# Performance work log

Hardware: AMD Instinct MI355X
Metric: run time of the kernel (lower is better)

## Reference

```python
import jax, jax.numpy as jnp
import numpy as np

B, C, F, N = 8, 128, 16, 512  # batch, in_channels, frames, num_nodes


def setup_inputs() -> dict:
    key = jax.random.key(0)
    k = jax.random.split(key, 6)
    return {
        # uniform(0,1) -> all entries nonzero -> complete graph with self-loops
        "Y": jax.random.uniform(k[0], (B, F, N, N), dtype=jnp.float32),
        "infos": jax.random.normal(k[1], (B, C, F, N), dtype=jnp.float32),
        # denseLayer: Linear(3C, C) -> weight [C, 3C], bias [C]
        "W_dense": jax.random.normal(k[2], (C, 3 * C), dtype=jnp.float32) / np.sqrt(3 * C).astype(np.float32),
        "b_dense": jax.random.normal(k[3], (C,), dtype=jnp.float32) * 0.01,
        # NodeApplyModule linear: Linear(C, C)
        "W_node": jax.random.normal(k[4], (C, C), dtype=jnp.float32) / np.sqrt(C).astype(np.float32),
        "b_node": jax.random.normal(k[5], (C,), dtype=jnp.float32) * 0.01,
    }


def reference(Y, infos, W_dense, b_dense, W_node, b_node):
    Bs, Cs, Fs, Ns = infos.shape
    # graph_update: frame 0 uses Y[:,0], frames 1..11 use Y[:,1], frames >11 use Y[:,2]
    frames = jnp.arange(Fs)
    y_idx = jnp.where(frames == 0, 0, jnp.where(frames <= 11, 1, 2))
    M = (Y[:, y_idx] != 0).astype(infos.dtype)          # [B,F,N,N] adjacency mask (u->v)
    X = jnp.transpose(infos, (0, 2, 3, 1))               # [B,F,N,C] node features

    # msg(u,v) = X[u] * (cat[X[u], X[v], X[u]-X[v]] @ W_dense.T + b_dense)
    # Linear is separable: gate(u,v) = S[u] + D[v] + b_dense with
    #   S = X @ (W1+W3).T, D = X @ (W2-W3).T
    W1, W2, W3 = jnp.split(W_dense, 3, axis=1)           # each [C,C]
    S = jnp.einsum('bfnc,dc->bfnd', X, W1 + W3)
    D = jnp.einsum('bfnc,dc->bfnd', X, W2 - W3)

    # mean over incoming edges u of msg(u,v):
    #   sum_u M[u,v] * X[u]*S[u]  +  (sum_u M[u,v]*X[u]) * (D[v]+b)
    A1 = jnp.einsum('bfuv,bfuc->bfvc', M, X * S)
    A2 = jnp.einsum('bfuv,bfuc->bfvc', M, X)
    deg = jnp.maximum(M.sum(axis=2), 1.0)[..., None]     # in-degree [B,F,N,1]
    agg = (A1 + A2 * (D + b_dense)) / deg

    # NodeApplyModule: relu(Linear(agg))
    h = jax.nn.relu(jnp.einsum('bfnc,oc->bfno', agg, W_node) + b_node)
    # reshape/permute to [B, C, F, N] and final relu (idempotent after relu)
    return jax.nn.relu(jnp.transpose(h, (0, 3, 1, 2)))
```

## Files before the change

### kernel.cpp

```cpp
#include <hip/hip_runtime.h>
#include <hip/hip_bf16.h>

#define B_ 8
#define C_ 128
#define F_ 16
#define N_ 512
#define CAP_ (N_ * N_)

typedef __attribute__((ext_vector_type(8))) short bf16x8;
typedef __attribute__((ext_vector_type(4))) float f32x4;

#define MFMA(a, b, c) __builtin_amdgcn_mfma_f32_16x16x32_bf16((a), (b), (c), 0, 0, 0)
#define SWZ(x) ((x) ^ ((((x) >> 8) & 7) << 4))

__device__ __forceinline__ ushort f2bf(float x) {
    union { __hip_bfloat16 h; ushort u; } cv;
    cv.h = __float2bfloat16(x);
    return cv.u;
}

__global__ __launch_bounds__(256) void k_prep(
    const float* __restrict__ Y, const float* __restrict__ Wd, const float* __restrict__ Wn,
    float* __restrict__ deg, int* __restrict__ cnt, int* __restrict__ list,
    float* __restrict__ Wsum, float* __restrict__ Wdiff, float* __restrict__ WsumT,
    ushort* __restrict__ WdT_bf, float* __restrict__ WnT)
{
    int t = threadIdx.x;
    if (blockIdx.y == 8) {
        for (int i = blockIdx.x * 256 + t; i < C_ * C_; i += 24 * 256) {
            int d = i >> 7, c = i & 127;
            const float* row = Wd + (size_t)d * (3 * C_);
            float w1 = row[c], w2 = row[C_ + c], w3 = row[2 * C_ + c];
            float ws = w1 + w3, wdf = w2 - w3;
            Wsum[i] = ws;
            Wdiff[i] = wdf;
            WsumT[(size_t)c * C_ + d] = ws;
            WdT_bf[(size_t)c * C_ + d] = f2bf(wdf);
            WnT[i] = Wn[(size_t)(i & 127) * C_ + (i >> 7)];
        }
        return;
    }
    __shared__ float red0[256], red1[256];
    int bg = blockIdx.x, vc = blockIdx.y;
    int b = bg / 3, g = bg % 3;
    int p = t & 31, q = t >> 5;
    int v = vc * 64 + p * 2;
    const float* Yp = Y + ((size_t)b * F_ + g) * N_ * N_;
    float d0 = 0.f, d1 = 0.f;
    #pragma unroll 4
    for (int i = 0; i < 64; ++i) {
        int u = q * 64 + i;
        float2 a = *(const float2*)(Yp + (size_t)u * N_ + v);
        if (a.x == 0.f) {
            int idx = atomicAdd(&cnt[bg], 1);
            list[(size_t)bg * CAP_ + idx] = (u << 9) | v;
        } else d0 += 1.f;
        if (a.y == 0.f) {
            int idx = atomicAdd(&cnt[bg], 1);
            list[(size_t)bg * CAP_ + idx] = (u << 9) | (v + 1);
        } else d1 += 1.f;
    }
    red0[t] = d0;
    red1[t] = d1;
    __syncthreads();
    if (t < 32) {
        float s0 = 0.f, s1 = 0.f;
        #pragma unroll
        for (int qq = 0; qq < 8; ++qq) { s0 += red0[qq * 32 + t]; s1 += red1[qq * 32 + t]; }
        deg[(size_t)bg * N_ + vc * 64 + t * 2]     = s0;
        deg[(size_t)bg * N_ + vc * 64 + t * 2 + 1] = s1;
    }
}

__global__ __launch_bounds__(256) void k_gram(
    const float* __restrict__ infos, const float* __restrict__ WsumT,
    float* __restrict__ A1row, float* __restrict__ A2row)
{
    __shared__ float smf[8448];
    __shared__ float red[256];
    short* Xs = (short*)smf;
    float* Gl = smf;
    int bf = blockIdx.x, nh = blockIdx.y, t = threadIdx.x;
    int b = bf >> 4, f = bf & 15;
    const float* Xg = infos + ((size_t)b * C_ * F_ + f) * N_;

    float a2p0 = 0.f, a2p1 = 0.f, a2p2 = 0.f, a2p3 = 0.f;
    float4 pre0, pre1, pre2, pre3;
    int sc = t >> 3, suq = t & 7;

    auto LOADREG = [&](int ks) {
        int u0 = ks * 32;
        const float* pbase = Xg + (size_t)sc * (F_ * N_) + u0 + suq * 4;
        pre0 = *(const float4*)(pbase);
        pre1 = *(const float4*)(pbase + 32 * (F_ * N_));
        pre2 = *(const float4*)(pbase + 64 * (F_ * N_));
        pre3 = *(const float4*)(pbase + 96 * (F_ * N_));
    };
    auto WRITELDS = [&](int buf) {
        short* dst = &Xs[buf * 5120 + sc * 40 + suq * 4];
        float4 xs[4] = {pre0, pre1, pre2, pre3};
        #pragma unroll
        for (int it = 0; it < 4; ++it) {
            float4 x = xs[it];
            float s4 = x.x + x.y + x.z + x.w;
            if (it == 0) a2p0 += s4; else if (it == 1) a2p1 += s4;
            else if (it == 2) a2p2 += s4; else a2p3 += s4;
            short4 h;
            h.x = (short)f2bf(x.x); h.y = (short)f2bf(x.y);
            h.z = (short)f2bf(x.z); h.w = (short)f2bf(x.w);
            *(short4*)(dst + it * 32 * 40) = h;
        }
    };

    int l = t & 63, w = t >> 6;
    int r = l & 15, q = l >> 4;
    f32x4 acc[2][4];
    #pragma unroll
    for (int mi = 0; mi < 2; ++mi)
        #pragma unroll
        for (int ni = 0; ni < 4; ++ni) acc[mi][ni] = (f32x4){0.f, 0.f, 0.f, 0.f};

    LOADREG(0);
    WRITELDS(0);
    for (int ks = 0; ks < 16; ++ks) {
        __syncthreads();
        if (ks < 15) LOADREG(ks + 1);
        const short* Xb = &Xs[(ks & 1) * 5120];
        bf16x8 a0 = *(const bf16x8*)&Xb[(w * 32 + r) * 40 + q * 8];
        bf16x8 a1 = *(const bf16x8*)&Xb[(w * 32 + 16 + r) * 40 + q * 8];
        bf16x8 b0 = *(const bf16x8*)&Xb[(nh * 64 + 0  + r) * 40 + q * 8];
        bf16x8 b1 = *(const bf16x8*)&Xb[(nh * 64 + 16 + r) * 40 + q * 8];
        bf16x8 b2 = *(const bf16x8*)&Xb[(nh * 64 + 32 + r) * 40 + q * 8];
        bf16x8 b3 = *(const bf16x8*)&Xb[(nh * 64 + 48 + r) * 40 + q * 8];
        acc[0][0] = MFMA(a0, b0, acc[0][0]);
        acc[0][1] = MFMA(a0, b1, acc[0][1]);
        acc[0][2] = MFMA(a0, b2, acc[0][2]);
        acc[0][3] = MFMA(a0, b3, acc[0][3]);
        acc[1][0] = MFMA(a1, b0, acc[1][0]);
        acc[1][1] = MFMA(a1, b1, acc[1][1]);
        acc[1][2] = MFMA(a1, b2, acc[1][2]);
        acc[1][3] = MFMA(a1, b3, acc[1][3]);
        if (ks < 15) WRITELDS((ks + 1) & 1);
    }
    __syncthreads();
    #pragma unroll
    for (int mi = 0; mi < 2; ++mi)
        #pragma unroll
        for (int ni = 0; ni < 4; ++ni) {
            int cb = w * 32 + mi * 16 + q * 4;
            int dl = ni * 16 + r;
            #pragma unroll
            for (int j = 0; j < 4; ++j) Gl[(cb + j) * 66 + dl] = acc[mi][ni][j];
        }
    __syncthreads();
    {
        int dl = t & 63, cq = t >> 6;
        float pacc = 0.f;
        #pragma unroll 8
        for (int i = 0; i < 32; ++i) {
            int c = cq * 32 + i;
            pacc += WsumT[(size_t)c * C_ + nh * 64 + dl] * Gl[c * 66 + dl];
        }
        red[t] = pacc;
    }
    __syncthreads();
    if (t < 64)
        A1row[(size_t)bf * C_ + nh * 64 + t] = red[t] + red[t + 64] + red[t + 128] + red[t + 192];
    if (nh == 0) {
        #pragma unroll
        for (int it = 0; it < 4; ++it) {
            float v2 = (it == 0) ? a2p0 : (it == 1) ? a2p1 : (it == 2) ? a2p2 : a2p3;
            v2 += __shfl_xor(v2, 1);
            v2 += __shfl_xor(v2, 2);
            v2 += __shfl_xor(v2, 4);
            if ((t & 7) == 0) A2row[(size_t)bf * C_ + it * 32 + (t >> 3)] = v2;
        }
    }
}

__global__ __launch_bounds__(256) void k_meff(
    const float* __restrict__ A1row, const float* __restrict__ A2row,
    const float* __restrict__ Wn, const float* __restrict__ WnT,
    const ushort* __restrict__ WdT_bf, const float* __restrict__ bd,
    ushort* __restrict__ Meff_bf, float* __restrict__ c0all)
{
    __shared__ ushort Zl[16384];
    __shared__ ushort Wl[16384];
    __shared__ float A2l[C_], El[C_];
    int bf = blockIdx.x, t = threadIdx.x;
    if (t < C_) {
        float a2 = A2row[(size_t)bf * C_ + t];
        A2l[t] = a2;
        El[t] = A1row[(size_t)bf * C_ + t] + a2 * bd[t];
    }
    __syncthreads();
    #pragma unroll
    for (int it = 0; it < 8; ++it) {
        int idx = it * 256 + t;
        int rowi = idx >> 4, ch = idx & 15;
        bf16x8 wv = *(const bf16x8*)&WdT_bf[(size_t)rowi * C_ + ch * 8];
        *(bf16x8*)((char*)Wl + SWZ(rowi * 256 + ch * 16)) = wv;
        const float4 w0 = *(const float4*)&Wn[(size_t)rowi * C_ + ch * 8];
        const float4 w1 = *(const float4*)&Wn[(size_t)rowi * C_ + ch * 8 + 4];
        bf16x8 z;
        z[0] = (short)f2bf(w0.x * A2l[ch * 8 + 0]);
        z[1] = (short)f2bf(w0.y * A2l[ch * 8 + 1]);
        z[2] = (short)f2bf(w0.z * A2l[ch * 8 + 2]);
        z[3] = (short)f2bf(w0.w * A2l[ch * 8 + 3]);
        z[4] = (short)f2bf(w1.x * A2l[ch * 8 + 4]);
        z[5] = (short)f2bf(w1.y * A2l[ch * 8 + 5]);
        z[6] = (short)f2bf(w1.z * A2l[ch * 8 + 6]);
        z[7] = (short)f2bf(w1.w * A2l[ch * 8 + 7]);
        *(bf16x8*)((char*)Zl + SWZ(rowi * 256 + ch * 16)) = z;
    }
    __syncthreads();
    int l = t & 63, w = t >> 6, r = l & 15, q = l >> 4;
    f32x4 acc[2][8];
    #pragma unroll
    for (int mi = 0; mi < 2; ++mi)
        #pragma unroll
        for (int ni = 0; ni < 8; ++ni) acc[mi][ni] = (f32x4){0.f, 0.f, 0.f, 0.f};
    #pragma unroll
    for (int ks = 0; ks < 4; ++ks) {
        int ko = ks * 64 + q * 16;
        bf16x8 a0 = *(const bf16x8*)((char*)Zl + SWZ((w * 32 + r) * 256 + ko));
        bf16x8 a1 = *(const bf16x8*)((char*)Zl + SWZ((w * 32 + 16 + r) * 256 + ko));
        #pragma unroll
        for (int ni = 0; ni < 8; ++ni) {
            bf16x8 bb = *(const bf16x8*)((char*)Wl + SWZ((ni * 16 + r) * 256 + ko));
            acc[0][ni] = MFMA(a0, bb, acc[0][ni]);
            acc[1][ni] = MFMA(a1, bb, acc[1][ni]);
        }
    }
    __syncthreads();
    #pragma unroll
    for (int mi = 0; mi < 2; ++mi)
        #pragma unroll
        for (int ni = 0; ni < 8; ++ni) {
            int o = w * 32 + mi * 16 + q * 4;
            int c = ni * 16 + r;
            #pragma unroll
            for (int j = 0; j < 4; ++j) Zl[(o + j) * C_ + c] = f2bf(acc[mi][ni][j]);
        }
    __syncthreads();
    #pragma unroll
    for (int it = 0; it < 8; ++it) {
        int idx = it * 256 + t;
        int rowi = idx >> 4, ch = idx & 15;
        *(bf16x8*)&Meff_bf[(size_t)bf * 16384 + rowi * C_ + ch * 8] =
            *(const bf16x8*)&Zl[rowi * C_ + ch * 8];
    }
    if (t < C_) {
        float s = 0.f;
        for (int c = 0; c < C_; ++c) s += WnT[(size_t)c * C_ + t] * El[c];
        c0all[(size_t)bf * C_ + t] = s;
    }
}

__global__ __launch_bounds__(256) void k_final(
    const float* __restrict__ infos, const ushort* __restrict__ Meff_bf,
    const float* __restrict__ c0all, const float* __restrict__ deg,
    const int* __restrict__ cnt, const int* __restrict__ list,
    const float* __restrict__ Wsum, const float* __restrict__ Wdiff,
    const float* __restrict__ Wn, const float* __restrict__ bd, const float* __restrict__ bn,
    float* __restrict__ out)
{
    __shared__ char arena[49152];
    ushort* Ml = (ushort*)arena;
    ushort* Xv = (ushort*)(arena + 32768);
    float*  Sl = (float*)arena;
    __shared__ float Xu[C_], Xvf[C_], NC[C_], corrv[C_];
    int bf = blockIdx.x, vb = blockIdx.y, t = threadIdx.x;
    int b = bf >> 4, f = bf & 15;
    int g = (f == 0) ? 0 : ((f <= 11) ? 1 : 2);
    int bg = b * 3 + g;
    int v0 = vb * 64;
    const float* Xg = infos + ((size_t)b * C_ * F_ + f) * N_;

    #pragma unroll
    for (int it = 0; it < 8; ++it) {
        int idx = it * 256 + t;
        int o = idx >> 4, ch = idx & 15;
        bf16x8 mv = *(const bf16x8*)&Meff_bf[(size_t)bf * 16384 + o * C_ + ch * 8];
        *(bf16x8*)((char*)Ml + SWZ(o * 256 + ch * 16)) = mv;
    }
    #pragma unroll
    for (int it = 0; it < 4; ++it) {
        int idx = it * 256 + t;
        int cp = idx >> 4, vq = idx & 15;
        const float* r0 = Xg + (size_t)(2 * cp) * (F_ * N_) + v0 + vq * 4;
        const float* r1 = r0 + (F_ * N_);
        float4 x0 = *(const float4*)r0;
        float4 x1 = *(const float4*)r1;
        float e0[4] = {x0.x, x0.y, x0.z, x0.w};
        float e1[4] = {x1.x, x1.y, x1.z, x1.w};
        #pragma unroll
        for (int j = 0; j < 4; ++j) {
            int vloc = vq * 4 + j;
            unsigned word = (unsigned)f2bf(e0[j]) | ((unsigned)f2bf(e1[j]) << 16);
            *(unsigned*)((char*)Xv + SWZ(vloc * 256 + cp * 4)) = word;
        }
    }
    __syncthreads();

    int l = t & 63, w = t >> 6, r = l & 15, q = l >> 4;
    f32x4 acc[2][4];
    #pragma unroll
    for (int mi = 0; mi < 2; ++mi)
        #pragma unroll
        for (int ni = 0; ni < 4; ++ni) acc[mi][ni] = (f32x4){0.f, 0.f, 0.f, 0.f};
    #pragma unroll
    for (int ks = 0; ks < 4; ++ks) {
        int ko = ks * 64 + q * 16;
        bf16x8 a0 = *(const bf16x8*)((char*)Ml + SWZ((w * 32 + r) * 256 + ko));
        bf16x8 a1 = *(const bf16x8*)((char*)Ml + SWZ((w * 32 + 16 + r) * 256 + ko));
        #pragma unroll
        for (int nt = 0; nt < 4; ++nt) {
            bf16x8 bb = *(const bf16x8*)((char*)Xv + SWZ((nt * 16 + r) * 256 + ko));
            acc[0][nt] = MFMA(a0, bb, acc[0][nt]);
            acc[1][nt] = MFMA(a1, bb, acc[1][nt]);
        }
    }

    int nz = cnt[bg];
    for (int e = 0; e < nz; ++e) {
        int p = list[(size_t)bg * CAP_ + e];
        int u = p >> 9, v = p & 511;
        if ((v >> 6) != vb) continue;
        int vloc = v - v0;
        __syncthreads();
        if (t < C_) {
            Xu[t]  = Xg[(size_t)t * (F_ * N_) + u];
            Xvf[t] = Xg[(size_t)t * (F_ * N_) + v];
        }
        __syncthreads();
        if (t < C_) {
            float s = 0.f, dv = 0.f;
            const float* wsr = Wsum + (size_t)t * C_;
            const float* wdr = Wdiff + (size_t)t * C_;
            for (int c = 0; c < C_; ++c) { s += wsr[c] * Xu[c]; dv += wdr[c] * Xvf[c]; }
            NC[t] = Xu[t] * (s + dv + bd[t]);
        }
        __syncthreads();
        if (t < C_) {
            float s = 0.f;
            const float* wnr = Wn + (size_t)t * C_;
            for (int c = 0; c < C_; ++c) s += wnr[c] * NC[c];
            corrv[t] = s;
        }
        __syncthreads();
        int ntv = vloc >> 4;
        #pragma unroll
        for (int nt = 0; nt < 4; ++nt) {
            if (nt == ntv && r == (vloc & 15)) {
                #pragma unroll
                for (int mi = 0; mi < 2; ++mi)
                    #pragma unroll
                    for (int j = 0; j < 4; ++j)
                        acc[mi][nt][j] -= corrv[w * 32 + mi * 16 + q * 4 + j];
            }
        }
    }

    float c0v[2][4], bnv[2][4];
    #pragma unroll
    for (int mi = 0; mi < 2; ++mi)
        #pragma unroll
        for (int j = 0; j < 4; ++j) {
            int o = w * 32 + mi * 16 + q * 4 + j;
            c0v[mi][j] = c0all[(size_t)bf * C_ + o];
            bnv[mi][j] = bn[o];
        }
    __syncthreads();
    #pragma unroll
    for (int nt = 0; nt < 4; ++nt) {
        int v = v0 + nt * 16 + r;
        float dg = fmaxf(deg[(size_t)bg * N_ + v], 1.f);
        #pragma unroll
        for (int mi = 0; mi < 2; ++mi) {
            int o = w * 32 + mi * 16 + q * 4;
            #pragma unroll
            for (int j = 0; j < 4; ++j) {
                float val = fmaxf((acc[mi][nt][j] + c0v[mi][j]) / dg + bnv[mi][j], 0.f);
                Sl[(o + j) * 66 + nt * 16 + r] = val;
            }
        }
    }
    __syncthreads();
    {
        int o = t >> 1, half = t & 1;
        float* src = &Sl[o * 66 + half * 32];
        float* dst = &out[((size_t)b * C_ + o) * (F_ * N_) + (size_t)f * N_ + v0 + half * 32];
        #pragma unroll
        for (int j = 0; j < 8; ++j)
            *(float4*)(dst + j * 4) = *(const float4*)(src + j * 4);
    }
}

extern "C" void kernel_launch(void* const* d_in, const int* in_sizes, int n_in,
                              void* d_out, int out_size, void* d_ws, size_t ws_size,
                              hipStream_t stream)
{
    const float* Y     = (const float*)d_in[0];
    const float* infos = (const float*)d_in[1];
    const float* Wd    = (const float*)d_in[2];
    const float* bd    = (const float*)d_in[3];
    const float* Wn    = (const float*)d_in[4];
    const float* bn    = (const float*)d_in[5];
    float* out = (float*)d_out;
    float* ws  = (float*)d_ws;

    float*  deg     = ws;
    int*    cnt     = (int*)(ws + 12288);
    float*  A1row   = ws + 12320;
    float*  A2row   = A1row + 16384;
    float*  Wsum    = A2row + 16384;
    float*  Wdiff   = Wsum + 16384;
    float*  WsumT   = Wdiff + 16384;
    float*  WnT     = WsumT + 16384;
    float*  c0all   = WnT + 16384;
    ushort* WdT_bf  = (ushort*)(c0all + 16384);
    ushort* Meff_bf = (ushort*)(c0all + 16384 + 8192);
    int*    list    = (int*)(c0all + 16384 + 8192 + 1048576);

    hipMemsetAsync(cnt, 0, 32 * sizeof(int), stream);
    k_prep<<<dim3(24, 9), 256, 0, stream>>>(Y, Wd, Wn, deg, cnt, list,
                                            Wsum, Wdiff, WsumT, WdT_bf, WnT);
    k_gram<<<dim3(B_ * F_, 2), 256, 0, stream>>>(infos, WsumT, A1row, A2row);
    k_meff<<<B_ * F_, 256, 0, stream>>>(A1row, A2row, Wn, WnT, WdT_bf, bd, Meff_bf, c0all);
    k_final<<<dim3(B_ * F_, 8), 256, 0, stream>>>(infos, Meff_bf, c0all, deg, cnt, list,
                                                  Wsum, Wdiff, Wn, bd, bn, out);
}
```

Measured before the change: 284.1 us.

## Fuse gram and Meff kernels into one 512-thread block per frame

Merges the Gram-matrix/A1/A2 kernel and the Meff kernel into a single 512-thread kernel per (batch, frame). A1 and A2 are reduced in shared memory instead of round-tripping through global memory, which removes one launch. WdT and Meff operands are now read straight from global memory instead of being staged in LDS. The final kernel likewise reads Meff directly from global, shrinking its LDS arena, which may help occupancy but adds uncoalesced global loads. The fused kernel runs only 128 blocks, so the Gram work is no longer split across two blocks per frame.

```diff
diff --git a/kernel.cpp b/kernel.cpp
--- a/kernel.cpp
+++ b/kernel.cpp
@@ -72,136 +72,90 @@
     }
 }
 
-__global__ __launch_bounds__(256) void k_gram(
+__global__ __launch_bounds__(512) void k_gram_meff(
     const float* __restrict__ infos, const float* __restrict__ WsumT,
-    float* __restrict__ A1row, float* __restrict__ A2row)
-{
-    __shared__ float smf[8448];
-    __shared__ float red[256];
-    short* Xs = (short*)smf;
-    float* Gl = smf;
-    int bf = blockIdx.x, nh = blockIdx.y, t = threadIdx.x;
-    int b = bf >> 4, f = bf & 15;
-    const float* Xg = infos + ((size_t)b * C_ * F_ + f) * N_;
-
-    float a2p0 = 0.f, a2p1 = 0.f, a2p2 = 0.f, a2p3 = 0.f;
-    float4 pre0, pre1, pre2, pre3;
-    int sc = t >> 3, suq = t & 7;
-
-    auto LOADREG = [&](int ks) {
-        int u0 = ks * 32;
-        const float* pbase = Xg + (size_t)sc * (F_ * N_) + u0 + suq * 4;
-        pre0 = *(const float4*)(pbase);
-        pre1 = *(const float4*)(pbase + 32 * (F_ * N_));
-        pre2 = *(const float4*)(pbase + 64 * (F_ * N_));
-        pre3 = *(const float4*)(pbase + 96 * (F_ * N_));
-    };
-    auto WRITELDS = [&](int buf) {
-        short* dst = &Xs[buf * 5120 + sc * 40 + suq * 4];
-        float4 xs[4] = {pre0, pre1, pre2, pre3};
-        #pragma unroll
-        for (int it = 0; it < 4; ++it) {
-            float4 x = xs[it];
-            float s4 = x.x + x.y + x.z + x.w;
-            if (it == 0) a2p0 += s4; else if (it == 1) a2p1 += s4;
-            else if (it == 2) a2p2 += s4; else a2p3 += s4;
-            short4 h;
-            h.x = (short)f2bf(x.x); h.y = (short)f2bf(x.y);
-            h.z = (short)f2bf(x.z); h.w = (short)f2bf(x.w);
-            *(short4*)(dst + it * 32 * 40) = h;
-        }
-    };
-
-    int l = t & 63, w = t >> 6;
-    int r = l & 15, q = l >> 4;
-    f32x4 acc[2][4];
-    #pragma unroll
-    for (int mi = 0; mi < 2; ++mi)
-        #pragma unroll
-        for (int ni = 0; ni < 4; ++ni) acc[mi][ni] = (f32x4){0.f, 0.f, 0.f, 0.f};
-
-    LOADREG(0);
-    WRITELDS(0);
-    for (int ks = 0; ks < 16; ++ks) {
-        __syncthreads();
-        if (ks < 15) LOADREG(ks + 1);
-        const short* Xb = &Xs[(ks & 1) * 5120];
-        bf16x8 a0 = *(const bf16x8*)&Xb[(w * 32 + r) * 40 + q * 8];
-        bf16x8 a1 = *(const bf16x8*)&Xb[(w * 32 + 16 + r) * 40 + q * 8];
-        bf16x8 b0 = *(const bf16x8*)&Xb[(nh * 64 + 0  + r) * 40 + q * 8];
-        bf16x8 b1 = *(const bf16x8*)&Xb[(nh * 64 + 16 + r) * 40 + q * 8];
-        bf16x8 b2 = *(const bf16x8*)&Xb[(nh * 64 + 32 + r) * 40 + q * 8];
-        bf16x8 b3 = *(const bf16x8*)&Xb[(nh * 64 + 48 + r) * 40 + q * 8];
-        acc[0][0] = MFMA(a0, b0, acc[0][0]);
-        acc[0][1] = MFMA(a0, b1, acc[0][1]);
-        acc[0][2] = MFMA(a0, b2, acc[0][2]);
-        acc[0][3] = MFMA(a0, b3, acc[0][3]);
-        acc[1][0] = MFMA(a1, b0, acc[1][0]);
-        acc[1][1] = MFMA(a1, b1, acc[1][1]);
-        acc[1][2] = MFMA(a1, b2, acc[1][2]);
-        acc[1][3] = MFMA(a1, b3, acc[1][3]);
-        if (ks < 15) WRITELDS((ks + 1) & 1);
-    }
-    __syncthreads();
-    #pragma unroll
-    for (int mi = 0; mi < 2; ++mi)
-        #pragma unroll
-        for (int ni = 0; ni < 4; ++ni) {
-            int cb = w * 32 + mi * 16 + q * 4;
-            int dl = ni * 16 + r;
-            #pragma unroll
-            for (int j = 0; j < 4; ++j) Gl[(cb + j) * 66 + dl] = acc[mi][ni][j];
-        }
-    __syncthreads();
-    {
-        int dl = t & 63, cq = t >> 6;
-        float pacc = 0.f;
-        #pragma unroll 8
-        for (int i = 0; i < 32; ++i) {
-            int c = cq * 32 + i;
-            pacc += WsumT[(size_t)c * C_ + nh * 64 + dl] * Gl[c * 66 + dl];
-        }
-        red[t] = pacc;
-    }
-    __syncthreads();
-    if (t < 64)
-        A1row[(size_t)bf * C_ + nh * 64 + t] = red[t] + red[t + 64] + red[t + 128] + red[t + 192];
-    if (nh == 0) {
-        #pragma unroll
-        for (int it = 0; it < 4; ++it) {
-            float v2 = (it == 0) ? a2p0 : (it == 1) ? a2p1 : (it == 2) ? a2p2 : a2p3;
-            v2 += __shfl_xor(v2, 1);
-            v2 += __shfl_xor(v2, 2);
-            v2 += __shfl_xor(v2, 4);
-            if ((t & 7) == 0) A2row[(size_t)bf * C_ + it * 32 + (t >> 3)] = v2;
-        }
-    }
-}
-
-__global__ __launch_bounds__(256) void k_meff(
-    const float* __restrict__ A1row, const float* __restrict__ A2row,
     const float* __restrict__ Wn, const float* __restrict__ WnT,
     const ushort* __restrict__ WdT_bf, const float* __restrict__ bd,
     ushort* __restrict__ Meff_bf, float* __restrict__ c0all)
 {
-    __shared__ ushort Zl[16384];
-    __shared__ ushort Wl[16384];
+    __shared__ char arena[32768];
+    short*  Xs = (short*)arena;
+    ushort* Zl = (ushort*)arena;
+    __shared__ float A1red[8][132];
+    __shared__ float A2red[512];
     __shared__ float A2l[C_], El[C_];
     int bf = blockIdx.x, t = threadIdx.x;
+    int b = bf >> 4, f = bf & 15;
+    const float* Xg = infos + ((size_t)b * C_ * F_ + f) * N_;
+
+    int sc = t >> 2, suq = t & 3;
+    float a2p = 0.f;
+    float4 pre0, pre1;
+    auto LOADREG = [&](int ks) {
+        const float* p = Xg + (size_t)sc * (F_ * N_) + ks * 32 + suq * 4;
+        pre0 = *(const float4*)p;
+        pre1 = *(const float4*)(p + 16);
+    };
+    auto WRITELDS = [&](int buf) {
+        a2p += pre0.x + pre0.y + pre0.z + pre0.w + pre1.x + pre1.y + pre1.z + pre1.w;
+        short4 h0, h1;
+        h0.x = (short)f2bf(pre0.x); h0.y = (short)f2bf(pre0.y);
+        h0.z = (short)f2bf(pre0.z); h0.w = (short)f2bf(pre0.w);
+        h1.x = (short)f2bf(pre1.x); h1.y = (short)f2bf(pre1.y);
+        h1.z = (short)f2bf(pre1.z); h1.w = (short)f2bf(pre1.w);
+        *(short4*)&Xs[buf * 5120 + sc * 40 + suq * 4]        = h0;
+        *(short4*)&Xs[buf * 5120 + sc * 40 + (suq + 4) * 4]  = h1;
+    };
+
+    int l = t & 63, w = t >> 6;
+    int r = l & 15, q = l >> 4;
+    f32x4 acc[8];
+    #pragma unroll
+    for (int ni = 0; ni < 8; ++ni) acc[ni] = (f32x4){0.f, 0.f, 0.f, 0.f};
+
+    LOADREG(0);
+    WRITELDS(0);
+    for (int ks = 0; ks < 16; ++ks) {
+        __syncthreads();
+        if (ks < 15) LOADREG(ks + 1);
+        const short* Xb = &Xs[(ks & 1) * 5120];
+        bf16x8 av = *(const bf16x8*)&Xb[(w * 16 + r) * 40 + q * 8];
+        #pragma unroll
+        for (int ni = 0; ni < 8; ++ni) {
+            bf16x8 bv = *(const bf16x8*)&Xb[(ni * 16 + r) * 40 + q * 8];
+            acc[ni] = MFMA(av, bv, acc[ni]);
+        }
+        if (ks < 15) WRITELDS((ks + 1) & 1);
+    }
+    __syncthreads();
+    A2red[t] = a2p;
+    #pragma unroll
+    for (int ni = 0; ni < 8; ++ni) {
+        int dl = ni * 16 + r;
+        float p1 = 0.f;
+        #pragma unroll
+        for (int j = 0; j < 4; ++j)
+            p1 += WsumT[(size_t)(w * 16 + q * 4 + j) * C_ + dl] * acc[ni][j];
+        p1 += __shfl_xor(p1, 16);
+        p1 += __shfl_xor(p1, 32);
+        if (q == 0) A1red[w][dl] = p1;
+    }
+    __syncthreads();
     if (t < C_) {
-        float a2 = A2row[(size_t)bf * C_ + t];
+        float a1 = 0.f;
+        #pragma unroll
+        for (int w8 = 0; w8 < 8; ++w8) a1 += A1red[w8][t];
+        float a2 = A2red[t * 4] + A2red[t * 4 + 1] + A2red[t * 4 + 2] + A2red[t * 4 + 3];
         A2l[t] = a2;
-        El[t] = A1row[(size_t)bf * C_ + t] + a2 * bd[t];
-    }
-    __syncthreads();
-    #pragma unroll
-    for (int it = 0; it < 8; ++it) {
-        int idx = it * 256 + t;
-        int rowi = idx >> 4, ch = idx & 15;
-        bf16x8 wv = *(const bf16x8*)&WdT_bf[(size_t)rowi * C_ + ch * 8];
-        *(bf16x8*)((char*)Wl + SWZ(rowi * 256 + ch * 16)) = wv;
-        const float4 w0 = *(const float4*)&Wn[(size_t)rowi * C_ + ch * 8];
-        const float4 w1 = *(const float4*)&Wn[(size_t)rowi * C_ + ch * 8 + 4];
+        El[t] = a1 + a2 * bd[t];
+    }
+    __syncthreads();
+    #pragma unroll
+    for (int it = 0; it < 4; ++it) {
+        int idx = it * 512 + t;
+        int o = idx >> 4, ch = idx & 15;
+        const float4 w0 = *(const float4*)&Wn[(size_t)o * C_ + ch * 8];
+        const float4 w1 = *(const float4*)&Wn[(size_t)o * C_ + ch * 8 + 4];
         bf16x8 z;
         z[0] = (short)f2bf(w0.x * A2l[ch * 8 + 0]);
         z[1] = (short)f2bf(w0.y * A2l[ch * 8 + 1]);
@@ -211,41 +165,33 @@
         z[5] = (short)f2bf(w1.y * A2l[ch * 8 + 5]);
         z[6] = (short)f2bf(w1.z * A2l[ch * 8 + 6]);
         z[7] = (short)f2bf(w1.w * A2l[ch * 8 + 7]);
-        *(bf16x8*)((char*)Zl + SWZ(rowi * 256 + ch * 16)) = z;
-    }
-    __syncthreads();
-    int l = t & 63, w = t >> 6, r = l & 15, q = l >> 4;
-    f32x4 acc[2][8];
-    #pragma unroll
-    for (int mi = 0; mi < 2; ++mi)
-        #pragma unroll
-        for (int ni = 0; ni < 8; ++ni) acc[mi][ni] = (f32x4){0.f, 0.f, 0.f, 0.f};
+        *(bf16x8*)((char*)Zl + SWZ(o * 256 + ch * 16)) = z;
+    }
+    __syncthreads();
+    f32x4 acc2[8];
+    #pragma unroll
+    for (int ni = 0; ni < 8; ++ni) acc2[ni] = (f32x4){0.f, 0.f, 0.f, 0.f};
     #pragma unroll
     for (int ks = 0; ks < 4; ++ks) {
-        int ko = ks * 64 + q * 16;
-        bf16x8 a0 = *(const bf16x8*)((char*)Zl + SWZ((w * 32 + r) * 256 + ko));
-        bf16x8 a1 = *(const bf16x8*)((char*)Zl + SWZ((w * 32 + 16 + r) * 256 + ko));
+        bf16x8 av = *(const bf16x8*)((char*)Zl + SWZ((w * 16 + r) * 256 + ks * 64 + q * 16));
         #pragma unroll
         for (int ni = 0; ni < 8; ++ni) {
-            bf16x8 bb = *(const bf16x8*)((char*)Wl + SWZ((ni * 16 + r) * 256 + ko));
-            acc[0][ni] = MFMA(a0, bb, acc[0][ni]);
-            acc[1][ni] = MFMA(a1, bb, acc[1][ni]);
-        }
-    }
-    __syncthreads();
-    #pragma unroll
-    for (int mi = 0; mi < 2; ++mi)
-        #pragma unroll
-        for (int ni = 0; ni < 8; ++ni) {
-            int o = w * 32 + mi * 16 + q * 4;
-            int c = ni * 16 + r;
-            #pragma unroll
-            for (int j = 0; j < 4; ++j) Zl[(o + j) * C_ + c] = f2bf(acc[mi][ni][j]);
-        }
-    __syncthreads();
-    #pragma unroll
-    for (int it = 0; it < 8; ++it) {
-        int idx = it * 256 + t;
+            bf16x8 bv = *(const bf16x8*)&WdT_bf[(size_t)(ni * 16 + r) * C_ + ks * 32 + q * 8];
+            acc2[ni] = MFMA(av, bv, acc2[ni]);
+        }
+    }
+    __syncthreads();
+    #pragma unroll
+    for (int ni = 0; ni < 8; ++ni) {
+        int o = w * 16 + q * 4;
+        int c = ni * 16 + r;
+        #pragma unroll
+        for (int j = 0; j < 4; ++j) Zl[(o + j) * C_ + c] = f2bf(acc2[ni][j]);
+    }
+    __syncthreads();
+    #pragma unroll
+    for (int it = 0; it < 4; ++it) {
+        int idx = it * 512 + t;
         int rowi = idx >> 4, ch = idx & 15;
         *(bf16x8*)&Meff_bf[(size_t)bf * 16384 + rowi * C_ + ch * 8] =
             *(const bf16x8*)&Zl[rowi * C_ + ch * 8];
@@ -265,9 +211,8 @@
     const float* __restrict__ Wn, const float* __restrict__ bd, const float* __restrict__ bn,
     float* __restrict__ out)
 {
-    __shared__ char arena[49152];
-    ushort* Ml = (ushort*)arena;
-    ushort* Xv = (ushort*)(arena + 32768);
+    __shared__ char arena[33792];
+    ushort* Xv = (ushort*)arena;
     float*  Sl = (float*)arena;
     __shared__ float Xu[C_], Xvf[C_], NC[C_], corrv[C_];
     int bf = blockIdx.x, vb = blockIdx.y, t = threadIdx.x;
@@ -276,14 +221,8 @@
     int bg = b * 3 + g;
     int v0 = vb * 64;
     const float* Xg = infos + ((size_t)b * C_ * F_ + f) * N_;
-
-    #pragma unroll
-    for (int it = 0; it < 8; ++it) {
-        int idx = it * 256 + t;
-        int o = idx >> 4, ch = idx & 15;
-        bf16x8 mv = *(const bf16x8*)&Meff_bf[(size_t)bf * 16384 + o * C_ + ch * 8];
-        *(bf16x8*)((char*)Ml + SWZ(o * 256 + ch * 16)) = mv;
-    }
+    const ushort* Meffp = Meff_bf + (size_t)bf * 16384;
+
     #pragma unroll
     for (int it = 0; it < 4; ++it) {
         int idx = it * 256 + t;
@@ -311,12 +250,12 @@
         for (int ni = 0; ni < 4; ++ni) acc[mi][ni] = (f32x4){0.f, 0.f, 0.f, 0.f};
     #pragma unroll
     for (int ks = 0; ks < 4; ++ks) {
-        int ko = ks * 64 + q * 16;
-        bf16x8 a0 = *(const bf16x8*)((char*)Ml + SWZ((w * 32 + r) * 256 + ko));
-        bf16x8 a1 = *(const bf16x8*)((char*)Ml + SWZ((w * 32 + 16 + r) * 256 + ko));
+        int ke = ks * 32 + q * 8;
+        bf16x8 a0 = *(const bf16x8*)&Meffp[(size_t)(w * 32 + r) * C_ + ke];
+        bf16x8 a1 = *(const bf16x8*)&Meffp[(size_t)(w * 32 + 16 + r) * C_ + ke];
         #pragma unroll
         for (int nt = 0; nt < 4; ++nt) {
-            bf16x8 bb = *(const bf16x8*)((char*)Xv + SWZ((nt * 16 + r) * 256 + ko));
+            bf16x8 bb = *(const bf16x8*)((char*)Xv + SWZ((nt * 16 + r) * 256 + ks * 64 + q * 16));
             acc[0][nt] = MFMA(a0, bb, acc[0][nt]);
             acc[1][nt] = MFMA(a1, bb, acc[1][nt]);
         }
@@ -412,9 +351,7 @@
 
     float*  deg     = ws;
     int*    cnt     = (int*)(ws + 12288);
-    float*  A1row   = ws + 12320;
-    float*  A2row   = A1row + 16384;
-    float*  Wsum    = A2row + 16384;
+    float*  Wsum    = ws + 12320;
     float*  Wdiff   = Wsum + 16384;
     float*  WsumT   = Wdiff + 16384;
     float*  WnT     = WsumT + 16384;
@@ -426,8 +363,8 @@
     hipMemsetAsync(cnt, 0, 32 * sizeof(int), stream);
     k_prep<<<dim3(24, 9), 256, 0, stream>>>(Y, Wd, Wn, deg, cnt, list,
                                             Wsum, Wdiff, WsumT, WdT_bf, WnT);
-    k_gram<<<dim3(B_ * F_, 2), 256, 0, stream>>>(infos, WsumT, A1row, A2row);
-    k_meff<<<B_ * F_, 256, 0, stream>>>(A1row, A2row, Wn, WnT, WdT_bf, bd, Meff_bf, c0all);
+    k_gram_meff<<<B_ * F_, 512, 0, stream>>>(infos, WsumT, Wn, WnT, WdT_bf, bd,
+                                             Meff_bf, c0all);
     k_final<<<dim3(B_ * F_, 8), 256, 0, stream>>>(infos, Meff_bf, c0all, deg, cnt, list,
                                                   Wsum, Wdiff, Wn, bd, bn, out);
 }
```

New measurement: 286.8 us. About the same (+1.0%).
